# Kernel tuning notes

Hardware: AMD Instinct MI355X
Metric: run time of the kernel (lower is better)

The kernel has to match this reference:

```python
import jax, jax.numpy as jnp
import numpy as np

CUBE = (80, 80, 20)
NBINS = CUBE[0] * CUBE[1] * CUBE[2]  # 128000
NVIEW = 5
B = 2
C_IMG, C_FEAT = 3, 32
H_IMG, W_IMG = 512, 512
H_F, W_F = 128, 128
HID = 256
IN_DIM = 3 + 2 * (C_IMG + C_FEAT)  # 73


def setup_inputs() -> dict:
    key = jax.random.key(0)
    ks = jax.random.split(key, 8)
    denorm_imgs = jax.random.uniform(ks[0], (NVIEW, B, C_IMG, H_IMG, W_IMG), jnp.float32)
    feats2d = jax.random.normal(ks[1], (NVIEW, B, C_FEAT, H_F, W_F), jnp.float32)
    # grid_sample coords in [-1, 1], last dim = (x, y)
    sample_grid = jax.random.uniform(ks[2], (NVIEW, NBINS, 2), jnp.float32, -1.0, 1.0)
    points = jax.random.normal(ks[3], (NBINS, 3), jnp.float32)
    W1 = jax.random.normal(ks[4], (IN_DIM, HID), jnp.float32) * (1.0 / np.sqrt(IN_DIM))
    b1 = jnp.zeros((HID,), jnp.float32)
    W2 = jax.random.normal(ks[5], (HID, 1), jnp.float32) * (1.0 / np.sqrt(HID))
    b2 = jnp.zeros((1,), jnp.float32)
    return {"denorm_imgs": denorm_imgs, "feats2d": feats2d, "sample_grid": sample_grid,
            "points": points, "W1": W1, "b1": b1, "W2": W2, "b2": b2}


def _grid_sample(img, grid):
    """Bilinear grid_sample, align_corners=True, padding_mode='zeros'.
    img: [B, C, H, W]; grid: [N, 2] in [-1, 1] (x, y). Returns [B, C, N]."""
    H, W = img.shape[-2], img.shape[-1]
    ix = (grid[:, 0] + 1.0) * 0.5 * (W - 1)
    iy = (grid[:, 1] + 1.0) * 0.5 * (H - 1)
    x0 = jnp.floor(ix)
    y0 = jnp.floor(iy)
    x1 = x0 + 1.0
    y1 = y0 + 1.0
    wx1 = ix - x0
    wx0 = 1.0 - wx1
    wy1 = iy - y0
    wy0 = 1.0 - wy1

    def corner(x, y, w):
        valid = ((x >= 0) & (x <= W - 1) & (y >= 0) & (y <= H - 1)).astype(img.dtype)
        xi = jnp.clip(x, 0, W - 1).astype(jnp.int32)
        yi = jnp.clip(y, 0, H - 1).astype(jnp.int32)
        vals = img[:, :, yi, xi]  # [B, C, N]
        return vals * (w * valid)[None, None, :]

    return (corner(x0, y0, wx0 * wy0) + corner(x1, y0, wx1 * wy0)
            + corner(x0, y1, wx0 * wy1) + corner(x1, y1, wx1 * wy1))


def reference(denorm_imgs, feats2d, sample_grid, points, W1, b1, W2, b2):
    # Batched multi-view grid_sample: [V, B, C, N]
    cubes_img = jax.vmap(_grid_sample)(denorm_imgs, sample_grid)
    cubes_feat = jax.vmap(_grid_sample)(feats2d, sample_grid)
    cubes = jnp.concatenate([cubes_img, cubes_feat], axis=2)  # [V, B, C_tot, N]
    cubes = jnp.transpose(cubes, (1, 2, 3, 0))  # [B, C_tot, N, V]
    nview = cubes.shape[-1]
    mean = jnp.sum(cubes, axis=-1, keepdims=True) / nview          # [B, C, N, 1]
    var = jnp.sum((cubes - mean) ** 2, axis=-1, keepdims=True) / nview
    var = jnp.exp(-var)
    gvol = jnp.concatenate([mean[..., 0], var[..., 0]], axis=1)    # [B, 2C, N]
    feats = jnp.transpose(gvol, (0, 2, 1))                         # [B, N, 2C]
    bsz = feats.shape[0]
    pts = jnp.broadcast_to(points[None], (bsz,) + points.shape)    # [B, N, 3]
    inp = jnp.concatenate([pts, feats], axis=-1)                   # [B, N, 3+2C]
    h = jax.nn.relu(inp @ W1 + b1)
    density = jax.nn.softplus(h @ W2 + b2)                         # [B, N, 1]
    alpha = 1.0 - jnp.exp(-density)
    return alpha.reshape(bsz, 1, CUBE[0], CUBE[1], CUBE[2])
```

## Files before the change

kernel.cpp:

```cpp
#include <hip/hip_runtime.h>

#define NVIEW 5
#define NB    128000
#define CF    32
#define HID   256
#define KA    96
#define IMG_HW 262144
#define FT_HW  16384

typedef __attribute__((ext_vector_type(8))) short short8;
typedef __attribute__((ext_vector_type(4))) float f32x4;
typedef __attribute__((ext_vector_type(2))) float f32x2;

__device__ __forceinline__ unsigned int f2bf(float f) {
    unsigned int u = __float_as_uint(f);
    return (u + 0x7fffu + ((u >> 16) & 1u)) >> 16;
}
__device__ __forceinline__ unsigned int pk(float a, float b) {
    return f2bf(a) | (f2bf(b) << 16);
}
__device__ __forceinline__ float b2f_lo(unsigned int u) { return __uint_as_float(u << 16); }
__device__ __forceinline__ float b2f_hi(unsigned int u) { return __uint_as_float(u & 0xffff0000u); }

__device__ __forceinline__ int mapk(int k) {
    if (k < 3)  return k + 3;
    if (k < 6)  return k + 35;
    if (k < 14) return k;
    if (k < 22) return k + 27;
    if (k < 24) return -1;
    if (k < 32) return k - 10;
    if (k < 40) return k + 17;
    if (k < 48) return -1;
    if (k < 56) return k - 26;
    if (k < 64) return k + 1;
    if (k < 72) return -1;
    if (k < 80) return k - 42;
    if (k < 88) return k - 15;
    if (k < 91) return k - 88;
    return -1;
}

__global__ __launch_bounds__(256) void prep(
    const float* __restrict__ imgs, const float* __restrict__ feats,
    const float* __restrict__ W1, const float* __restrict__ b1,
    const float* __restrict__ W2, const float* __restrict__ b2,
    uint2* __restrict__ imgsP, uint4* __restrict__ featsP,
    unsigned int* __restrict__ Bfrag, float* __restrict__ bw)
{
    const int bidx = blockIdx.x;
    const int t = threadIdx.x;
    if (bidx < 1280) {
        int gid = bidx * 256 + t;
        int v   = gid >> 16;
        int px  = (gid & 65535) * 4;
        const float* base = imgs + (size_t)v * 6 * IMG_HW + px;
        float4 pl[6];
        #pragma unroll
        for (int p = 0; p < 6; p++)
            pl[p] = *(const float4*)(base + (size_t)p * IMG_HW);
        uint2 o[4];
        #pragma unroll
        for (int i = 0; i < 4; i++) {
            unsigned int c[6];
            #pragma unroll
            for (int p = 0; p < 6; p++)
                c[p] = (unsigned int)fminf(((const float*)&pl[p])[i] * 255.f + 0.5f, 255.f);
            o[i].x = c[0] | (c[1] << 8) | (c[2] << 16);
            o[i].y = c[3] | (c[4] << 8) | (c[5] << 16);
        }
        uint4* dst = (uint4*)(imgsP + (size_t)v * IMG_HW + px);
        dst[0] = make_uint4(o[0].x, o[0].y, o[1].x, o[1].y);
        dst[1] = make_uint4(o[2].x, o[2].y, o[3].x, o[3].y);
    } else if (bidx < 2560) {
        __shared__ __align__(16) unsigned short tile[64][68];
        const int pixbase = (bidx - 1280) * 64;
        const int v   = pixbase >> 14;
        const int rem = pixbase & 16383;
        {
            #pragma unroll
            for (int it = 0; it < 4; it++) {
                int idx   = it * 256 + t;
                int plane = idx >> 4;
                int px4   = (idx & 15) * 4;
                float4 f = *(const float4*)(feats + ((size_t)v * 64 + plane) * FT_HW + rem + px4);
                ushort4 o;
                o.x = (unsigned short)f2bf(f.x);
                o.y = (unsigned short)f2bf(f.y);
                o.z = (unsigned short)f2bf(f.z);
                o.w = (unsigned short)f2bf(f.w);
                *(ushort4*)&tile[plane][px4] = o;
            }
        }
        __syncthreads();
        {
            const int q = t & 7;
            #pragma unroll
            for (int it = 0; it < 2; it++) {
                int p = it * 32 + (t >> 3);
                uint4 o;
                o.x = (unsigned)tile[q * 8 + 0][p] | ((unsigned)tile[q * 8 + 1][p] << 16);
                o.y = (unsigned)tile[q * 8 + 2][p] | ((unsigned)tile[q * 8 + 3][p] << 16);
                o.z = (unsigned)tile[q * 8 + 4][p] | ((unsigned)tile[q * 8 + 5][p] << 16);
                o.w = (unsigned)tile[q * 8 + 6][p] | ((unsigned)tile[q * 8 + 7][p] << 16);
                featsP[(size_t)(pixbase + p) * 8 + q] = o;
            }
        }
    } else {
        int e = (bidx - 2560) * 256 + t;
        int ju = e & 3;
        int nn = (e >> 2) & 255;
        int o  = e >> 10;
        int k0 = o * 8 + ju * 2;
        int i0 = mapk(k0), i1 = mapk(k0 + 1);
        float f0 = (i0 >= 0) ? W1[i0 * 256 + nn] : 0.f;
        float f1 = (i1 >= 0) ? W1[i1 * 256 + nn] : 0.f;
        Bfrag[e] = pk(f0, f1);
        if (e < 256)       bw[e] = b1[e];
        else if (e < 512)  bw[e] = W2[e - 256];
        else if (e == 512) bw[e] = b2[0];
    }
}

#define AROW 13

__global__ __launch_bounds__(256, 4) void fused_gather_mlp(
    const uint2* __restrict__ imgsP,
    const unsigned short* __restrict__ featsP,
    const float* __restrict__ grid,
    const float* __restrict__ points,
    const unsigned int*   __restrict__ Bfrag,
    const float*          __restrict__ bw,
    float* __restrict__ out)
{
    __shared__ unsigned int Lds[3328];
    __shared__ float b1s[HID];
    __shared__ float W2s[HID];

    const int tid = threadIdx.x;
    b1s[tid] = bw[tid];
    W2s[tid] = bw[256 + tid];
    const float b2v = bw[512];

    const int n = blockIdx.x * 32 + (tid >> 3);
    const int b = (tid >> 2) & 1;
    const int q = tid & 3;
    const int qxi = q & 1;
    const int qyi = q >> 1;
    const float qxf = (float)qxi;
    const float qyf = (float)qyi;

    f32x2 sum2[4], ssq2[4];
    #pragma unroll
    for (int d = 0; d < 4; d++) { sum2[d] = (f32x2){0.f, 0.f}; ssq2[d] = (f32x2){0.f, 0.f}; }
    float si0 = 0.f, si1 = 0.f, si2 = 0.f;
    float qi0 = 0.f, qi1 = 0.f, qi2 = 0.f;
    float p0 = 0.f, p1 = 0.f, p2 = 0.f;
    if (q == 3) {
        p0 = points[n * 3 + 0];
        p1 = points[n * 3 + 1];
        p2 = points[n * 3 + 2];
    }

    const uint4* fbase = (const uint4*)featsP + (size_t)b * 4 + q;

    #pragma unroll
    for (int v = 0; v < NVIEW; v++) {
        const float2 g = ((const float2*)grid)[v * NB + n];
        const float gx = g.x, gy = g.y;

        {
            float ix = (gx + 1.f) * 0.5f * 511.f;
            float iy = (gy + 1.f) * 0.5f * 511.f;
            float x0f = floorf(ix), y0f = floorf(iy);
            float wx1 = ix - x0f, wx0 = 1.f - wx1;
            float wy1 = iy - y0f, wy0 = 1.f - wy1;
            float wx = qxi ? wx1 : wx0;
            float wy = qyi ? wy1 : wy0;
            bool okx = qxi ? (x0f >= -1.f && x0f <= 510.f) : (x0f >= 0.f && x0f <= 511.f);
            bool oky = qyi ? (y0f >= -1.f && y0f <= 510.f) : (y0f >= 0.f && y0f <= 511.f);
            float wk = (okx && oky) ? wx * wy : 0.f;
            int xi = (int)fminf(fmaxf(x0f + qxf, 0.f), 511.f);
            int yi = (int)fminf(fmaxf(y0f + qyf, 0.f), 511.f);
            uint2 iv = imgsP[(size_t)v * IMG_HW + yi * 512 + xi];
            unsigned sel = b ? iv.y : iv.x;
            float c0 = wk * (float)(sel & 255u);
            float c1 = wk * (float)((sel >> 8) & 255u);
            float c2 = wk * (float)((sel >> 16) & 255u);
            c0 += __shfl_xor(c0, 1); c1 += __shfl_xor(c1, 1); c2 += __shfl_xor(c2, 1);
            c0 += __shfl_xor(c0, 2); c1 += __shfl_xor(c1, 2); c2 += __shfl_xor(c2, 2);
            si0 += c0; qi0 += c0 * c0;
            si1 += c1; qi1 += c1 * c1;
            si2 += c2; qi2 += c2 * c2;
        }

        {
            float ix = (gx + 1.f) * 0.5f * 127.f;
            float iy = (gy + 1.f) * 0.5f * 127.f;
            float x0f = floorf(ix), y0f = floorf(iy);
            float wx1 = ix - x0f, wx0 = 1.f - wx1;
            float wy1 = iy - y0f, wy0 = 1.f - wy1;
            wx0 = (x0f >= 0.f && x0f <= 127.f) ? wx0 : 0.f;
            wx1 = (x0f >= -1.f && x0f <= 126.f) ? wx1 : 0.f;
            wy0 = (y0f >= 0.f && y0f <= 127.f) ? wy0 : 0.f;
            wy1 = (y0f >= -1.f && y0f <= 126.f) ? wy1 : 0.f;
            float w00 = wx0 * wy0, w01 = wx1 * wy0, w10 = wx0 * wy1, w11 = wx1 * wy1;
            int xi0 = (int)fminf(fmaxf(x0f,       0.f), 127.f);
            int xi1 = (int)fminf(fmaxf(x0f + 1.f, 0.f), 127.f);
            int r0  = (int)fminf(fmaxf(y0f,       0.f), 127.f) * 128;
            int r1  = (int)fminf(fmaxf(y0f + 1.f, 0.f), 127.f) * 128;
            const uint4* fb = fbase + (size_t)v * (FT_HW * 8);
            uint4 c00 = fb[(size_t)(r0 + xi0) * 8];
            uint4 c01 = fb[(size_t)(r0 + xi1) * 8];
            uint4 c10 = fb[(size_t)(r1 + xi0) * 8];
            uint4 c11 = fb[(size_t)(r1 + xi1) * 8];
            const unsigned int* u00 = (const unsigned int*)&c00;
            const unsigned int* u01 = (const unsigned int*)&c01;
            const unsigned int* u10 = (const unsigned int*)&c10;
            const unsigned int* u11 = (const unsigned int*)&c11;
            #pragma unroll
            for (int d = 0; d < 4; d++) {
                f32x2 a00 = {b2f_lo(u00[d]), b2f_hi(u00[d])};
                f32x2 a01 = {b2f_lo(u01[d]), b2f_hi(u01[d])};
                f32x2 a10 = {b2f_lo(u10[d]), b2f_hi(u10[d])};
                f32x2 a11 = {b2f_lo(u11[d]), b2f_hi(u11[d])};
                f32x2 val = w00 * a00 + w01 * a01 + w10 * a10 + w11 * a11;
                sum2[d] += val;
                ssq2[d] += val * val;
            }
        }
    }

    float sumf[8], ssqf[8];
    #pragma unroll
    for (int d = 0; d < 4; d++) {
        sumf[2 * d]     = sum2[d][0];
        sumf[2 * d + 1] = sum2[d][1];
        ssqf[2 * d]     = ssq2[d][0];
        ssqf[2 * d + 1] = ssq2[d][1];
    }
    #pragma unroll
    for (int c = 0; c < 8; c++) {
        float m = sumf[c] * 0.2f;
        float qq = ssqf[c] * 0.2f - m * m;
        sumf[c] = m;
        ssqf[c] = __expf(-qq);
    }
    const float s1 = 0.2f * (1.f / 255.f);
    const float s2 = 0.2f * (1.f / 65025.f);
    float mi0 = si0 * s1, mi1 = si1 * s1, mi2 = si2 * s1;
    float ei0 = __expf(-(qi0 * s2 - mi0 * mi0));
    float ei1 = __expf(-(qi1 * s2 - mi1 * mi1));
    float ei2 = __expf(-(qi2 * s2 - mi2 * mi2));

    unsigned int u[12];
    if (q == 0) {
        u[0] = pk(mi0, mi1);
        u[1] = pk(mi2, ei0);
        u[2] = pk(ei1, ei2);
        #pragma unroll
        for (int j = 0; j < 4; j++) u[3 + j] = pk(sumf[2 * j], sumf[2 * j + 1]);
        #pragma unroll
        for (int j = 0; j < 4; j++) u[7 + j] = pk(ssqf[2 * j], ssqf[2 * j + 1]);
        u[11] = 0u;
    } else {
        #pragma unroll
        for (int j = 0; j < 4; j++) u[j]     = pk(sumf[2 * j], sumf[2 * j + 1]);
        #pragma unroll
        for (int j = 0; j < 4; j++) u[4 + j] = pk(ssqf[2 * j], ssqf[2 * j + 1]);
        u[8] = 0u; u[9] = 0u; u[10] = 0u; u[11] = 0u;
        if (q == 3) { u[8] = pk(p0, p1); u[9] = pk(p2, 0.f); }
    }

    uint4* As4 = (uint4*)Lds;
    {
        uint4* arow = &As4[(tid >> 2) * AROW + q * 3];
        #pragma unroll
        for (int i = 0; i < 3; i++)
            arow[i] = make_uint4(u[4 * i], u[4 * i + 1], u[4 * i + 2], u[4 * i + 3]);
    }

    const int w    = tid >> 6;
    const int lane = tid & 63;
    const int col  = lane & 15;
    const int quad = lane >> 4;
    const long rowbase = (long)blockIdx.x * 64 + w * 16;

    short8 af[3];
    #pragma unroll
    for (int s = 0; s < 3; s++)
        af[s] = *(const short8*)&As4[(w * 16 + col) * AROW + s * 4 + quad];

    __syncthreads();

    float pm[4] = {0.f, 0.f, 0.f, 0.f};
    #pragma unroll
    for (int qb = 0; qb < 4; qb++) {
        {
            const uint4* src = (const uint4*)Bfrag;
            uint4* dst = (uint4*)Lds;
            #pragma unroll
            for (int i = 0; i < 3; i++) {
                int g = i * 256 + tid;
                dst[g] = src[(g >> 8) * 1024 + ((g >> 6) & 3) * 256 + qb * 64 + (g & 63)];
            }
        }
        __syncthreads();

        f32x4 acc[4];
        #pragma unroll
        for (int tt = 0; tt < 4; tt++)
            acc[tt] = (f32x4){0.f, 0.f, 0.f, 0.f};

        const unsigned int* bp = Lds + quad * 256 + col * 4;
        #pragma unroll
        for (int s = 0; s < 3; s++) {
            #pragma unroll
            for (int tt = 0; tt < 4; tt++) {
                short8 bf = *(const short8*)(bp + s * 1024 + tt * 64);
                acc[tt] = __builtin_amdgcn_mfma_f32_16x16x32_bf16(af[s], bf, acc[tt], 0, 0, 0);
            }
        }

        #pragma unroll
        for (int tt = 0; tt < 4; tt++) {
            int j = (qb * 4 + tt) * 16 + col;
            float b1v = b1s[j];
            float w2v = W2s[j];
            #pragma unroll
            for (int r = 0; r < 4; r++) {
                float hh = fmaxf(acc[tt][r] + b1v, 0.f);
                pm[r] += hh * w2v;
            }
        }
        if (qb < 3) __syncthreads();
    }

    #pragma unroll
    for (int r = 0; r < 4; r++) {
        float p = pm[r];
        p += __shfl_xor(p, 1);
        p += __shfl_xor(p, 2);
        p += __shfl_xor(p, 4);
        p += __shfl_xor(p, 8);
        pm[r] = p;
    }

    if (col == 0) {
        #pragma unroll
        for (int r = 0; r < 4; r++) {
            float x  = pm[r] + b2v;
            float sp = fmaxf(x, 0.f) + log1pf(expf(-fabsf(x)));
            float alpha = -expm1f(-sp);
            long row = rowbase + quad * 4 + r;
            out[(row & 1) * (long)NB + (row >> 1)] = alpha;
        }
    }
}

extern "C" void kernel_launch(void* const* d_in, const int* in_sizes, int n_in,
                              void* d_out, int out_size, void* d_ws, size_t ws_size,
                              hipStream_t stream) {
    const float* imgs   = (const float*)d_in[0];
    const float* feats  = (const float*)d_in[1];
    const float* grid   = (const float*)d_in[2];
    const float* points = (const float*)d_in[3];
    const float* W1     = (const float*)d_in[4];
    const float* b1     = (const float*)d_in[5];
    const float* W2     = (const float*)d_in[6];
    const float* b2     = (const float*)d_in[7];
    float* out = (float*)d_out;

    uint2*          imgsP  = (uint2*)d_ws;
    unsigned short* featsP = (unsigned short*)(imgsP + (size_t)NVIEW * IMG_HW);
    unsigned int*   Bfrag  = (unsigned int*)(featsP + (size_t)NVIEW * FT_HW * 64);
    float*          bwbuf  = (float*)(Bfrag + 12288);

    prep<<<dim3(2608), dim3(256), 0, stream>>>(
        imgs, feats, W1, b1, W2, b2,
        imgsP, (uint4*)featsP, Bfrag, bwbuf);
    fused_gather_mlp<<<dim3(4000), dim3(256), 0, stream>>>(
        imgsP, featsP, grid, points, Bfrag, bwbuf, out);
}
```

Measured before the change: 177.4 us.

## Software-pipeline multi-view gathers and relax launch bounds for more registers

Loads all five grid coordinates up front, issues all image-pixel gathers together, and double-buffers the feature-map corner gathers so the loads for view v+2 are in flight while view v is accumulated. This is meant to raise memory-level parallelism and hide gather latency. The launch bound drops from 4 to 2 waves-per-SIMD hint to leave room for the extra live registers. The cost is possibly lower occupancy, which may cancel part of the latency hiding.

```diff
diff --git a/kernel.cpp b/kernel.cpp
--- a/kernel.cpp
+++ b/kernel.cpp
@@ -123,7 +123,7 @@
 
 #define AROW 13
 
-__global__ __launch_bounds__(256, 4) void fused_gather_mlp(
+__global__ __launch_bounds__(256, 2) void fused_gather_mlp(
     const uint2* __restrict__ imgsP,
     const unsigned short* __restrict__ featsP,
     const float* __restrict__ grid,
@@ -163,72 +163,88 @@
 
     const uint4* fbase = (const uint4*)featsP + (size_t)b * 4 + q;
 
+    float2 g[NVIEW];
+    #pragma unroll
+    for (int v = 0; v < NVIEW; v++)
+        g[v] = ((const float2*)grid)[v * NB + n];
+
+    uint2 ivv[NVIEW];
+    float wki[NVIEW];
     #pragma unroll
     for (int v = 0; v < NVIEW; v++) {
-        const float2 g = ((const float2*)grid)[v * NB + n];
-        const float gx = g.x, gy = g.y;
-
-        {
-            float ix = (gx + 1.f) * 0.5f * 511.f;
-            float iy = (gy + 1.f) * 0.5f * 511.f;
-            float x0f = floorf(ix), y0f = floorf(iy);
-            float wx1 = ix - x0f, wx0 = 1.f - wx1;
-            float wy1 = iy - y0f, wy0 = 1.f - wy1;
-            float wx = qxi ? wx1 : wx0;
-            float wy = qyi ? wy1 : wy0;
-            bool okx = qxi ? (x0f >= -1.f && x0f <= 510.f) : (x0f >= 0.f && x0f <= 511.f);
-            bool oky = qyi ? (y0f >= -1.f && y0f <= 510.f) : (y0f >= 0.f && y0f <= 511.f);
-            float wk = (okx && oky) ? wx * wy : 0.f;
-            int xi = (int)fminf(fmaxf(x0f + qxf, 0.f), 511.f);
-            int yi = (int)fminf(fmaxf(y0f + qyf, 0.f), 511.f);
-            uint2 iv = imgsP[(size_t)v * IMG_HW + yi * 512 + xi];
-            unsigned sel = b ? iv.y : iv.x;
-            float c0 = wk * (float)(sel & 255u);
-            float c1 = wk * (float)((sel >> 8) & 255u);
-            float c2 = wk * (float)((sel >> 16) & 255u);
-            c0 += __shfl_xor(c0, 1); c1 += __shfl_xor(c1, 1); c2 += __shfl_xor(c2, 1);
-            c0 += __shfl_xor(c0, 2); c1 += __shfl_xor(c1, 2); c2 += __shfl_xor(c2, 2);
-            si0 += c0; qi0 += c0 * c0;
-            si1 += c1; qi1 += c1 * c1;
-            si2 += c2; qi2 += c2 * c2;
-        }
-
-        {
-            float ix = (gx + 1.f) * 0.5f * 127.f;
-            float iy = (gy + 1.f) * 0.5f * 127.f;
-            float x0f = floorf(ix), y0f = floorf(iy);
-            float wx1 = ix - x0f, wx0 = 1.f - wx1;
-            float wy1 = iy - y0f, wy0 = 1.f - wy1;
-            wx0 = (x0f >= 0.f && x0f <= 127.f) ? wx0 : 0.f;
-            wx1 = (x0f >= -1.f && x0f <= 126.f) ? wx1 : 0.f;
-            wy0 = (y0f >= 0.f && y0f <= 127.f) ? wy0 : 0.f;
-            wy1 = (y0f >= -1.f && y0f <= 126.f) ? wy1 : 0.f;
-            float w00 = wx0 * wy0, w01 = wx1 * wy0, w10 = wx0 * wy1, w11 = wx1 * wy1;
-            int xi0 = (int)fminf(fmaxf(x0f,       0.f), 127.f);
-            int xi1 = (int)fminf(fmaxf(x0f + 1.f, 0.f), 127.f);
-            int r0  = (int)fminf(fmaxf(y0f,       0.f), 127.f) * 128;
-            int r1  = (int)fminf(fmaxf(y0f + 1.f, 0.f), 127.f) * 128;
-            const uint4* fb = fbase + (size_t)v * (FT_HW * 8);
-            uint4 c00 = fb[(size_t)(r0 + xi0) * 8];
-            uint4 c01 = fb[(size_t)(r0 + xi1) * 8];
-            uint4 c10 = fb[(size_t)(r1 + xi0) * 8];
-            uint4 c11 = fb[(size_t)(r1 + xi1) * 8];
-            const unsigned int* u00 = (const unsigned int*)&c00;
-            const unsigned int* u01 = (const unsigned int*)&c01;
-            const unsigned int* u10 = (const unsigned int*)&c10;
-            const unsigned int* u11 = (const unsigned int*)&c11;
-            #pragma unroll
-            for (int d = 0; d < 4; d++) {
-                f32x2 a00 = {b2f_lo(u00[d]), b2f_hi(u00[d])};
-                f32x2 a01 = {b2f_lo(u01[d]), b2f_hi(u01[d])};
-                f32x2 a10 = {b2f_lo(u10[d]), b2f_hi(u10[d])};
-                f32x2 a11 = {b2f_lo(u11[d]), b2f_hi(u11[d])};
-                f32x2 val = w00 * a00 + w01 * a01 + w10 * a10 + w11 * a11;
-                sum2[d] += val;
-                ssq2[d] += val * val;
-            }
-        }
-    }
+        float ix = (g[v].x + 1.f) * 0.5f * 511.f;
+        float iy = (g[v].y + 1.f) * 0.5f * 511.f;
+        float x0f = floorf(ix), y0f = floorf(iy);
+        float wx1 = ix - x0f, wx0 = 1.f - wx1;
+        float wy1 = iy - y0f, wy0 = 1.f - wy1;
+        float wx = qxi ? wx1 : wx0;
+        float wy = qyi ? wy1 : wy0;
+        bool okx = qxi ? (x0f >= -1.f && x0f <= 510.f) : (x0f >= 0.f && x0f <= 511.f);
+        bool oky = qyi ? (y0f >= -1.f && y0f <= 510.f) : (y0f >= 0.f && y0f <= 511.f);
+        wki[v] = (okx && oky) ? wx * wy : 0.f;
+        int xi = (int)fminf(fmaxf(x0f + qxf, 0.f), 511.f);
+        int yi = (int)fminf(fmaxf(y0f + qyf, 0.f), 511.f);
+        ivv[v] = imgsP[(size_t)v * IMG_HW + yi * 512 + xi];
+    }
+
+    auto featIssue = [&](float2 gg, const uint4* fb, uint4 (&c)[4], float (&wf)[4]) {
+        float ix = (gg.x + 1.f) * 0.5f * 127.f;
+        float iy = (gg.y + 1.f) * 0.5f * 127.f;
+        float x0f = floorf(ix), y0f = floorf(iy);
+        float wx1 = ix - x0f, wx0 = 1.f - wx1;
+        float wy1 = iy - y0f, wy0 = 1.f - wy1;
+        wx0 = (x0f >= 0.f && x0f <= 127.f) ? wx0 : 0.f;
+        wx1 = (x0f >= -1.f && x0f <= 126.f) ? wx1 : 0.f;
+        wy0 = (y0f >= 0.f && y0f <= 127.f) ? wy0 : 0.f;
+        wy1 = (y0f >= -1.f && y0f <= 126.f) ? wy1 : 0.f;
+        wf[0] = wx0 * wy0; wf[1] = wx1 * wy0; wf[2] = wx0 * wy1; wf[3] = wx1 * wy1;
+        int xi0 = (int)fminf(fmaxf(x0f,       0.f), 127.f);
+        int xi1 = (int)fminf(fmaxf(x0f + 1.f, 0.f), 127.f);
+        int r0  = (int)fminf(fmaxf(y0f,       0.f), 127.f) * 128;
+        int r1  = (int)fminf(fmaxf(y0f + 1.f, 0.f), 127.f) * 128;
+        c[0] = fb[(size_t)(r0 + xi0) * 8];
+        c[1] = fb[(size_t)(r0 + xi1) * 8];
+        c[2] = fb[(size_t)(r1 + xi0) * 8];
+        c[3] = fb[(size_t)(r1 + xi1) * 8];
+    };
+    auto featConsume = [&](uint4 (&c)[4], float (&wf)[4]) {
+        const unsigned int* u00 = (const unsigned int*)&c[0];
+        const unsigned int* u01 = (const unsigned int*)&c[1];
+        const unsigned int* u10 = (const unsigned int*)&c[2];
+        const unsigned int* u11 = (const unsigned int*)&c[3];
+        #pragma unroll
+        for (int d = 0; d < 4; d++) {
+            f32x2 a00 = {b2f_lo(u00[d]), b2f_hi(u00[d])};
+            f32x2 a01 = {b2f_lo(u01[d]), b2f_hi(u01[d])};
+            f32x2 a10 = {b2f_lo(u10[d]), b2f_hi(u10[d])};
+            f32x2 a11 = {b2f_lo(u11[d]), b2f_hi(u11[d])};
+            f32x2 val = wf[0] * a00 + wf[1] * a01 + wf[2] * a10 + wf[3] * a11;
+            sum2[d] += val;
+            ssq2[d] += val * val;
+        }
+    };
+    auto imgConsume = [&](uint2 iv, float wk) {
+        unsigned sel = b ? iv.y : iv.x;
+        float c0 = wk * (float)(sel & 255u);
+        float c1 = wk * (float)((sel >> 8) & 255u);
+        float c2 = wk * (float)((sel >> 16) & 255u);
+        c0 += __shfl_xor(c0, 1); c1 += __shfl_xor(c1, 1); c2 += __shfl_xor(c2, 1);
+        c0 += __shfl_xor(c0, 2); c1 += __shfl_xor(c1, 2); c2 += __shfl_xor(c2, 2);
+        si0 += c0; qi0 += c0 * c0;
+        si1 += c1; qi1 += c1 * c1;
+        si2 += c2; qi2 += c2 * c2;
+    };
+
+    uint4 cA[4], cB[4];
+    float wA[4], wB[4];
+    const size_t VSTRIDE = (size_t)FT_HW * 8;
+    featIssue(g[0], fbase + 0 * VSTRIDE, cA, wA);
+    featIssue(g[1], fbase + 1 * VSTRIDE, cB, wB);
+    featConsume(cA, wA); featIssue(g[2], fbase + 2 * VSTRIDE, cA, wA); imgConsume(ivv[0], wki[0]);
+    featConsume(cB, wB); featIssue(g[3], fbase + 3 * VSTRIDE, cB, wB); imgConsume(ivv[1], wki[1]);
+    featConsume(cA, wA); featIssue(g[4], fbase + 4 * VSTRIDE, cA, wA); imgConsume(ivv[2], wki[2]);
+    featConsume(cB, wB); imgConsume(ivv[3], wki[3]);
+    featConsume(cA, wA); imgConsume(ivv[4], wki[4]);
 
     float sumf[8], ssqf[8];
     #pragma unroll
@@ -300,8 +316,8 @@
             uint4* dst = (uint4*)Lds;
             #pragma unroll
             for (int i = 0; i < 3; i++) {
-                int g = i * 256 + tid;
-                dst[g] = src[(g >> 8) * 1024 + ((g >> 6) & 3) * 256 + qb * 64 + (g & 63)];
+                int gg = i * 256 + tid;
+                dst[gg] = src[(gg >> 8) * 1024 + ((gg >> 6) & 3) * 256 + qb * 64 + (gg & 63)];
             }
         }
         __syncthreads();
```

Result: faster. 173.3 us (-2.3%).
